# Optimization experiments

Measured on AMD Instinct MI355X. Metric: run time of the kernel, lower is better.

The kernel has to match this reference:

```python
import jax, jax.numpy as jnp
import numpy as np

N_QUBITS = 8
N_LAYERS = 2
DIM = 1 << N_QUBITS

# Precompute Pauli-Z eigenvalues per qubit (PennyLane: wire 0 = most significant bit)
_idx = np.arange(DIM)
_bits = ((_idx[None, :] >> (N_QUBITS - 1 - np.arange(N_QUBITS)[:, None])) & 1)  # [n, 2^n]
Z_EIG = jnp.asarray(1.0 - 2.0 * _bits, dtype=jnp.float32)                      # [n, 2^n]
# CZ diagonal signs for adjacent pairs (q, q+1)
CZ_SIGN = jnp.asarray(1.0 - 2.0 * (_bits[:-1] * _bits[1:]), dtype=jnp.float32)  # [n-1, 2^n]


def _rx(t):
    c = jnp.cos(0.5 * t).astype(jnp.complex64)
    s = jnp.sin(0.5 * t).astype(jnp.complex64)
    return jnp.stack([jnp.stack([c, -1j * s], -1), jnp.stack([-1j * s, c], -1)], -2)


def _ry(t):
    c = jnp.cos(0.5 * t).astype(jnp.complex64)
    s = jnp.sin(0.5 * t).astype(jnp.complex64)
    return jnp.stack([jnp.stack([c, -s], -1), jnp.stack([s, c], -1)], -2)


def _rz(t):
    e = jnp.exp(-0.5j * t.astype(jnp.complex64))
    z = jnp.zeros_like(e)
    return jnp.stack([jnp.stack([e, z], -1), jnp.stack([z, jnp.conj(e)], -1)], -2)


def _apply_1q(state, gate, q):
    # state: [B, 2^n]; gate: [B,2,2] (data-dependent angle) or [2,2] (shared weight)
    B = state.shape[0]
    L, R = 1 << q, 1 << (N_QUBITS - q - 1)
    st = state.reshape(B, L, 2, R)
    if gate.ndim == 3:
        st = jnp.einsum('bij,bljr->blir', gate, st)
    else:
        st = jnp.einsum('ij,bljr->blir', gate, st)
    return st.reshape(B, DIM)


def _circuit(angles, q_weights):
    # angles: [B, 3*n] real; q_weights: [n_layers, 2*n]
    B = angles.shape[0]
    state = jnp.zeros((B, DIM), dtype=jnp.complex64).at[:, 0].set(1.0)
    for l in range(N_LAYERS):
        for q in range(N_QUBITS):
            state = _apply_1q(state, _rx(angles[:, 3 * q]), q)
            state = _apply_1q(state, _ry(angles[:, 3 * q + 1]), q)
            state = _apply_1q(state, _rz(angles[:, 3 * q + 2]), q)
        for q in range(N_QUBITS):  # ansatz 1: hardware-efficient RY+RZ
            state = _apply_1q(state, _ry(q_weights[l, q]), q)
            state = _apply_1q(state, _rz(q_weights[l, q + N_QUBITS]), q)
        for q in range(N_QUBITS - 1):  # CZ chain (diagonal)
            state = state * CZ_SIGN[q]
    probs = state.real ** 2 + state.imag ** 2          # [B, 2^n]
    return probs @ Z_EIG.T                              # [B, n] expval PauliZ


def setup_inputs() -> dict:
    key = jax.random.key(0)
    ks = jax.random.split(key, 6)
    B = 8192
    return {
        'x': jax.random.normal(ks[0], (B, 64), dtype=jnp.float32),
        'W_adapter': jax.random.normal(ks[1], (3 * N_QUBITS, 64), dtype=jnp.float32) * 0.1,
        'b_adapter': jax.random.normal(ks[2], (3 * N_QUBITS,), dtype=jnp.float32) * 0.1,
        'q_weights': jax.random.normal(ks[3], (N_LAYERS, 2 * N_QUBITS), dtype=jnp.float32),
        'W_fc': jax.random.normal(ks[4], (1, N_QUBITS), dtype=jnp.float32) * 0.1,
        'b_fc': jax.random.normal(ks[5], (1,), dtype=jnp.float32) * 0.1,
    }


def reference(x, W_adapter, b_adapter, q_weights, W_fc, b_fc):
    angles = jnp.arctan(x @ W_adapter.T + b_adapter)   # [B, 3n]
    expvals = _circuit(angles, q_weights)              # [B, n]
    return expvals @ W_fc.T + b_fc                     # [B, 1]
```

## Files before the change

### kernel.cpp

```cpp
#include <hip/hip_runtime.h>
#include <math.h>

typedef __attribute__((ext_vector_type(2))) float f32x2;

__device__ __forceinline__ f32x2 sp(float s) { f32x2 v; v.x = s; v.y = s; return v; }

template <int CTRL, int RM, int BM>
__device__ __forceinline__ float dpp_add(float v) {
    int o = __builtin_amdgcn_update_dpp(0, __float_as_int(v), CTRL, RM, BM, true);
    return v + __int_as_float(o);
}

__device__ __forceinline__ float wave_total(float v) {
    v = dpp_add<0xB1, 0xF, 0xF>(v);
    v = dpp_add<0x4E, 0xF, 0xF>(v);
    v = dpp_add<0x114, 0xF, 0xE>(v);
    v = dpp_add<0x118, 0xF, 0xC>(v);
    v = dpp_add<0x142, 0xA, 0xF>(v);
    v = dpp_add<0x143, 0xC, 0xF>(v);
    return __int_as_float(__builtin_amdgcn_readlane(__float_as_int(v), 63));
}

__device__ __forceinline__ float read_lane(float v, int l) {
    return __int_as_float(__builtin_amdgcn_readlane(__float_as_int(v), l));
}

template <int P>
__device__ __forceinline__ float partner(float v) {
    int vi = __float_as_int(v);
    if constexpr (P == 0) {
        return __int_as_float(__builtin_amdgcn_update_dpp(vi, vi, 0xB1, 0xF, 0xF, false));
    } else if constexpr (P == 1) {
        return __int_as_float(__builtin_amdgcn_update_dpp(vi, vi, 0x4E, 0xF, 0xF, false));
    } else if constexpr (P == 2) {
        int a = __builtin_amdgcn_update_dpp(vi, vi, 0x104, 0xF, 0x5, false);
        a = __builtin_amdgcn_update_dpp(a, vi, 0x114, 0xF, 0xA, false);
        return __int_as_float(a);
    } else if constexpr (P == 3) {
        int a = __builtin_amdgcn_update_dpp(vi, vi, 0x108, 0xF, 0x3, false);
        a = __builtin_amdgcn_update_dpp(a, vi, 0x118, 0xF, 0xC, false);
        return __int_as_float(a);
    } else if constexpr (P == 4) {
        return __shfl_xor(v, 16, 64);
    } else {
        return __shfl_xor(v, 32, 64);
    }
}

template <int P>
__device__ __forceinline__ f32x2 partner2(f32x2 v) {
    f32x2 r; r.x = partner<P>(v.x); r.y = partner<P>(v.y); return r;
}

__device__ __forceinline__ void pair_gate(float& r0, float& i0, float& r1, float& i1,
                                          float ar, float ai, float br, float bi) {
    float nr0 = ar * r0 - ai * i0 - br * r1 - bi * i1;
    float ni0 = ar * i0 + ai * r0 + bi * r1 - br * i1;
    float nr1 = br * r0 - bi * i0 + ar * r1 + ai * i1;
    float ni1 = br * i0 + bi * r0 + ar * i1 - ai * r1;
    r0 = nr0; i0 = ni0; r1 = nr1; i1 = ni1;
}

__device__ __forceinline__ void pair_gate2(f32x2& r0, f32x2& i0, f32x2& r1, f32x2& i1,
                                           float ar, float ai, float br, float bi) {
    f32x2 va = sp(ar), vi = sp(ai), vb = sp(br), vc = sp(bi);
    f32x2 nr0 = va * r0 - vi * i0 - vb * r1 - vc * i1;
    f32x2 ni0 = va * i0 + vi * r0 + vc * r1 - vb * i1;
    f32x2 nr1 = vb * r0 - vc * i0 + va * r1 + vi * i1;
    f32x2 ni1 = vb * i0 + vc * r0 + va * i1 - vi * r1;
    r0 = nr0; i0 = ni0; r1 = nr1; i1 = ni1;
}

template <int P>
__device__ __forceinline__ void cross_gate(int lane, f32x2& Ar, f32x2& Ai, f32x2& Br, f32x2& Bi,
                                           float gar, float gai, float gbr, float gbi) {
    float sg = ((lane >> P) & 1) ? 1.0f : -1.0f;
    f32x2 vAr = sp(gar), vAi = sp(-sg * gai), vBr = sp(sg * gbr), vBi = sp(gbi);
    f32x2 pr = partner2<P>(Ar), pi = partner2<P>(Ai);
    f32x2 nAr = vAr * Ar - vAi * Ai + vBr * pr - vBi * pi;
    f32x2 nAi = vAr * Ai + vAi * Ar + vBr * pi + vBi * pr;
    Ar = nAr; Ai = nAi;
    pr = partner2<P>(Br); pi = partner2<P>(Bi);
    f32x2 nBr = vAr * Br - vAi * Bi + vBr * pr - vBi * pi;
    f32x2 nBi = vAr * Bi + vAi * Br + vBr * pi + vBi * pr;
    Br = nBr; Bi = nBi;
}

template <int G>
__device__ __forceinline__ void apply_g(int lane, f32x2& Ar, f32x2& Ai, f32x2& Br, f32x2& Bi,
                                        float garv, float gaiv, float gbrv, float gbiv) {
    constexpr int Q = G & 7;
    constexpr int P = 7 - Q;
    float ar = read_lane(garv, G), ai = read_lane(gaiv, G);
    float br = read_lane(gbrv, G), bi = read_lane(gbiv, G);
    if constexpr (P == 7) {
        pair_gate2(Ar, Ai, Br, Bi, ar, ai, br, bi);
    } else if constexpr (P == 6) {
        float r0 = Ar.x, i0 = Ai.x, r1 = Ar.y, i1 = Ai.y;
        pair_gate(r0, i0, r1, i1, ar, ai, br, bi);
        Ar.x = r0; Ai.x = i0; Ar.y = r1; Ai.y = i1;
        r0 = Br.x; i0 = Bi.x; r1 = Br.y; i1 = Bi.y;
        pair_gate(r0, i0, r1, i1, ar, ai, br, bi);
        Br.x = r0; Bi.x = i0; Br.y = r1; Bi.y = i1;
    } else {
        cross_gate<P>(lane, Ar, Ai, Br, Bi, ar, ai, br, bi);
    }
}

__global__ __launch_bounds__(256) void qcritic_kernel(
    const float* __restrict__ x,
    const float* __restrict__ Wad,
    const float* __restrict__ bad,
    const float* __restrict__ qw,
    const float* __restrict__ Wfc,
    const float* __restrict__ bfc,
    float* __restrict__ out,
    int B) {
    int tid = threadIdx.x;
    int lane = tid & 63;
    int b = blockIdx.x * 4 + (tid >> 6);
    if (b >= B) return;

    float xv = x[b * 64 + lane];
    float u[24];
#pragma unroll
    for (int j = 0; j < 24; ++j)
        u[j] = wave_total(xv * Wad[j * 64 + lane]) + bad[j];

    int Q = lane & 7;
    int L = (lane >> 3) & 1;
    bool b0 = Q & 1, b1 = Q & 2, b2 = Q & 4;
    float uq[3];
#pragma unroll
    for (int k = 0; k < 3; ++k) {
        float m01 = b0 ? u[3 + k] : u[0 + k];
        float m23 = b0 ? u[9 + k] : u[6 + k];
        float m45 = b0 ? u[15 + k] : u[12 + k];
        float m67 = b0 ? u[21 + k] : u[18 + k];
        float m03 = b1 ? m23 : m01;
        float m47 = b1 ? m67 : m45;
        uq[k] = b2 ? m47 : m03;
    }
    float ch[3], sh[3];
#pragma unroll
    for (int k = 0; k < 3; ++k) {
        float v = uq[k];
        float ct = rsqrtf(1.0f + v * v);
        ch[k] = sqrtf(0.5f * (1.0f + ct));
        sh[k] = __fdividef(0.5f * v * ct, ch[k]);
    }
    float cd, sd, wc, ws;
    __sincosf(0.5f * qw[(L << 4) + Q], &sd, &cd);
    __sincosf(0.5f * qw[(L << 4) + Q + 8], &ws, &wc);
    if (L == 1) { wc = 1.0f; ws = 0.0f; }
    float ca = ch[0], sa = sh[0], cb = ch[1], sb = sh[1], zc = ch[2], zs = sh[2];
    float pr = cb * ca, pi = sb * sa;
    float qr = sb * ca, qi = -cb * sa;
    float a1r = zc * pr + zs * pi, a1i = zc * pi - zs * pr;
    float b1r = zc * qr - zs * qi, b1i = zc * qi + zs * qr;
    float a2r = cd * a1r - sd * b1r, a2i = cd * a1i - sd * b1i;
    float b2r = sd * a1r + cd * b1r, b2i = sd * a1i + cd * b1i;
    float garv = wc * a2r + ws * a2i, gaiv = wc * a2i - ws * a2r;
    float gbrv = wc * b2r - ws * b2i, gbiv = wc * b2i + ws * b2r;

    f32x2 Ar, Ai, Br, Bi;
    Ar.x = (lane == 0) ? 1.0f : 0.0f; Ar.y = 0.0f;
    Ai = sp(0.0f); Br = sp(0.0f); Bi = sp(0.0f);

    f32x2 czA, czB;
    {
        int i0 = lane, i1 = 64 + lane, i2 = 128 + lane, i3 = 192 + lane;
        czA.x = (__popc(i0 & (i0 >> 1)) & 1) ? -1.0f : 1.0f;
        czA.y = (__popc(i1 & (i1 >> 1)) & 1) ? -1.0f : 1.0f;
        czB.x = (__popc(i2 & (i2 >> 1)) & 1) ? -1.0f : 1.0f;
        czB.y = (__popc(i3 & (i3 >> 1)) & 1) ? -1.0f : 1.0f;
    }

    apply_g<0>(lane, Ar, Ai, Br, Bi, garv, gaiv, gbrv, gbiv);
    apply_g<1>(lane, Ar, Ai, Br, Bi, garv, gaiv, gbrv, gbiv);
    apply_g<2>(lane, Ar, Ai, Br, Bi, garv, gaiv, gbrv, gbiv);
    apply_g<3>(lane, Ar, Ai, Br, Bi, garv, gaiv, gbrv, gbiv);
    apply_g<4>(lane, Ar, Ai, Br, Bi, garv, gaiv, gbrv, gbiv);
    apply_g<5>(lane, Ar, Ai, Br, Bi, garv, gaiv, gbrv, gbiv);
    apply_g<6>(lane, Ar, Ai, Br, Bi, garv, gaiv, gbrv, gbiv);
    apply_g<7>(lane, Ar, Ai, Br, Bi, garv, gaiv, gbrv, gbiv);
    Ar *= czA; Ai *= czA; Br *= czB; Bi *= czB;

    apply_g<8>(lane, Ar, Ai, Br, Bi, garv, gaiv, gbrv, gbiv);
    apply_g<9>(lane, Ar, Ai, Br, Bi, garv, gaiv, gbrv, gbiv);
    apply_g<10>(lane, Ar, Ai, Br, Bi, garv, gaiv, gbrv, gbiv);
    apply_g<11>(lane, Ar, Ai, Br, Bi, garv, gaiv, gbrv, gbiv);
    apply_g<12>(lane, Ar, Ai, Br, Bi, garv, gaiv, gbrv, gbiv);
    apply_g<13>(lane, Ar, Ai, Br, Bi, garv, gaiv, gbrv, gbiv);
    apply_g<14>(lane, Ar, Ai, Br, Bi, garv, gaiv, gbrv, gbiv);
    apply_g<15>(lane, Ar, Ai, Br, Bi, garv, gaiv, gbrv, gbiv);

    float glow = 0.0f;
#pragma unroll
    for (int k = 2; k < 8; ++k)
        glow += Wfc[k] * (((lane >> (7 - k)) & 1) ? -1.0f : 1.0f);
    float w0 = Wfc[0], w1 = Wfc[1];
    f32x2 gA, gB;
    gA.x = glow + w0 + w1; gA.y = glow + w0 - w1;
    gB.x = glow - w0 + w1; gB.y = glow - w0 - w1;
    f32x2 acc2 = (Ar * Ar + Ai * Ai) * gA + (Br * Br + Bi * Bi) * gB;
    float tot = wave_total(acc2.x + acc2.y);
    if (lane == 0) out[b] = tot + bfc[0];
}

extern "C" void kernel_launch(void* const* d_in, const int* in_sizes, int n_in,
                              void* d_out, int out_size, void* d_ws, size_t ws_size,
                              hipStream_t stream) {
    const float* x   = (const float*)d_in[0];
    const float* Wad = (const float*)d_in[1];
    const float* bad = (const float*)d_in[2];
    const float* qw  = (const float*)d_in[3];
    const float* Wfc = (const float*)d_in[4];
    const float* bfc = (const float*)d_in[5];
    float* out = (float*)d_out;
    int B = in_sizes[0] / 64;
    int grid = (B + 3) / 4;
    qcritic_kernel<<<grid, 256, 0, stream>>>(x, Wad, bad, qw, Wfc, bfc, out, B);
}
```

Before: 80.22 us.

## Add occupancy hint, hoist Wfc loads, move CZ sign compute, use precise math

Adds an 8-waves-per-EU launch bound and hoists the Wfc and bfc loads to the start of the kernel. It moves the CZ sign computation to the point where it is used, and makes the final reduction write from lane 63 instead of doing a readlane. It also swaps the fast intrinsics __sincosf and __fdividef for the precise sincosf and divide. The precise math paths cost more instructions, and the occupancy bound may force register spills.

```diff
diff --git a/kernel.cpp b/kernel.cpp
--- a/kernel.cpp
+++ b/kernel.cpp
@@ -11,14 +11,14 @@
     return v + __int_as_float(o);
 }
 
-__device__ __forceinline__ float wave_total(float v) {
+__device__ __forceinline__ float wave_sum63(float v) {
     v = dpp_add<0xB1, 0xF, 0xF>(v);
     v = dpp_add<0x4E, 0xF, 0xF>(v);
     v = dpp_add<0x114, 0xF, 0xE>(v);
     v = dpp_add<0x118, 0xF, 0xC>(v);
     v = dpp_add<0x142, 0xA, 0xF>(v);
     v = dpp_add<0x143, 0xC, 0xF>(v);
-    return __int_as_float(__builtin_amdgcn_readlane(__float_as_int(v), 63));
+    return v;
 }
 
 __device__ __forceinline__ float read_lane(float v, int l) {
@@ -107,7 +107,7 @@
     }
 }
 
-__global__ __launch_bounds__(256) void qcritic_kernel(
+__global__ __launch_bounds__(256, 8) void qcritic_kernel(
     const float* __restrict__ x,
     const float* __restrict__ Wad,
     const float* __restrict__ bad,
@@ -121,11 +121,20 @@
     int b = blockIdx.x * 4 + (tid >> 6);
     if (b >= B) return;
 
+    float w0 = Wfc[0], w1 = Wfc[1];
+    float glow = 0.0f;
+#pragma unroll
+    for (int k = 2; k < 8; ++k)
+        glow += Wfc[k] * (((lane >> (7 - k)) & 1) ? -1.0f : 1.0f);
+    float bfcv = bfc[0];
+
     float xv = x[b * 64 + lane];
-    float u[24];
-#pragma unroll
-    for (int j = 0; j < 24; ++j)
-        u[j] = wave_total(xv * Wad[j * 64 + lane]) + bad[j];
+    float su[24];
+#pragma unroll
+    for (int j = 0; j < 24; ++j) {
+        float p = wave_sum63(xv * Wad[j * 64 + lane]);
+        su[j] = read_lane(p, 63) + bad[j];
+    }
 
     int Q = lane & 7;
     int L = (lane >> 3) & 1;
@@ -133,10 +142,10 @@
     float uq[3];
 #pragma unroll
     for (int k = 0; k < 3; ++k) {
-        float m01 = b0 ? u[3 + k] : u[0 + k];
-        float m23 = b0 ? u[9 + k] : u[6 + k];
-        float m45 = b0 ? u[15 + k] : u[12 + k];
-        float m67 = b0 ? u[21 + k] : u[18 + k];
+        float m01 = b0 ? su[3 + k] : su[0 + k];
+        float m23 = b0 ? su[9 + k] : su[6 + k];
+        float m45 = b0 ? su[15 + k] : su[12 + k];
+        float m67 = b0 ? su[21 + k] : su[18 + k];
         float m03 = b1 ? m23 : m01;
         float m47 = b1 ? m67 : m45;
         uq[k] = b2 ? m47 : m03;
@@ -147,17 +156,17 @@
         float v = uq[k];
         float ct = rsqrtf(1.0f + v * v);
         ch[k] = sqrtf(0.5f * (1.0f + ct));
-        sh[k] = __fdividef(0.5f * v * ct, ch[k]);
+        sh[k] = 0.5f * v * ct / ch[k];
     }
     float cd, sd, wc, ws;
-    __sincosf(0.5f * qw[(L << 4) + Q], &sd, &cd);
-    __sincosf(0.5f * qw[(L << 4) + Q + 8], &ws, &wc);
+    sincosf(0.5f * qw[(L << 4) + Q], &sd, &cd);
+    sincosf(0.5f * qw[(L << 4) + Q + 8], &ws, &wc);
     if (L == 1) { wc = 1.0f; ws = 0.0f; }
     float ca = ch[0], sa = sh[0], cb = ch[1], sb = sh[1], zc = ch[2], zs = sh[2];
     float pr = cb * ca, pi = sb * sa;
-    float qr = sb * ca, qi = -cb * sa;
+    float qr = sb * ca, qi2 = -cb * sa;
     float a1r = zc * pr + zs * pi, a1i = zc * pi - zs * pr;
-    float b1r = zc * qr - zs * qi, b1i = zc * qi + zs * qr;
+    float b1r = zc * qr - zs * qi2, b1i = zc * qi2 + zs * qr;
     float a2r = cd * a1r - sd * b1r, a2i = cd * a1i - sd * b1i;
     float b2r = sd * a1r + cd * b1r, b2i = sd * a1i + cd * b1i;
     float garv = wc * a2r + ws * a2i, gaiv = wc * a2i - ws * a2r;
@@ -166,15 +175,6 @@
     f32x2 Ar, Ai, Br, Bi;
     Ar.x = (lane == 0) ? 1.0f : 0.0f; Ar.y = 0.0f;
     Ai = sp(0.0f); Br = sp(0.0f); Bi = sp(0.0f);
-
-    f32x2 czA, czB;
-    {
-        int i0 = lane, i1 = 64 + lane, i2 = 128 + lane, i3 = 192 + lane;
-        czA.x = (__popc(i0 & (i0 >> 1)) & 1) ? -1.0f : 1.0f;
-        czA.y = (__popc(i1 & (i1 >> 1)) & 1) ? -1.0f : 1.0f;
-        czB.x = (__popc(i2 & (i2 >> 1)) & 1) ? -1.0f : 1.0f;
-        czB.y = (__popc(i3 & (i3 >> 1)) & 1) ? -1.0f : 1.0f;
-    }
 
     apply_g<0>(lane, Ar, Ai, Br, Bi, garv, gaiv, gbrv, gbiv);
     apply_g<1>(lane, Ar, Ai, Br, Bi, garv, gaiv, gbrv, gbiv);
@@ -184,7 +184,16 @@
     apply_g<5>(lane, Ar, Ai, Br, Bi, garv, gaiv, gbrv, gbiv);
     apply_g<6>(lane, Ar, Ai, Br, Bi, garv, gaiv, gbrv, gbiv);
     apply_g<7>(lane, Ar, Ai, Br, Bi, garv, gaiv, gbrv, gbiv);
-    Ar *= czA; Ai *= czA; Br *= czB; Bi *= czB;
+
+    {
+        int i0 = lane, i1 = 64 + lane, i2 = 128 + lane, i3 = 192 + lane;
+        f32x2 czA, czB;
+        czA.x = (__popc(i0 & (i0 >> 1)) & 1) ? -1.0f : 1.0f;
+        czA.y = (__popc(i1 & (i1 >> 1)) & 1) ? -1.0f : 1.0f;
+        czB.x = (__popc(i2 & (i2 >> 1)) & 1) ? -1.0f : 1.0f;
+        czB.y = (__popc(i3 & (i3 >> 1)) & 1) ? -1.0f : 1.0f;
+        Ar *= czA; Ai *= czA; Br *= czB; Bi *= czB;
+    }
 
     apply_g<8>(lane, Ar, Ai, Br, Bi, garv, gaiv, gbrv, gbiv);
     apply_g<9>(lane, Ar, Ai, Br, Bi, garv, gaiv, gbrv, gbiv);
@@ -195,17 +204,12 @@
     apply_g<14>(lane, Ar, Ai, Br, Bi, garv, gaiv, gbrv, gbiv);
     apply_g<15>(lane, Ar, Ai, Br, Bi, garv, gaiv, gbrv, gbiv);
 
-    float glow = 0.0f;
-#pragma unroll
-    for (int k = 2; k < 8; ++k)
-        glow += Wfc[k] * (((lane >> (7 - k)) & 1) ? -1.0f : 1.0f);
-    float w0 = Wfc[0], w1 = Wfc[1];
     f32x2 gA, gB;
     gA.x = glow + w0 + w1; gA.y = glow + w0 - w1;
     gB.x = glow - w0 + w1; gB.y = glow - w0 - w1;
     f32x2 acc2 = (Ar * Ar + Ai * Ai) * gA + (Br * Br + Bi * Bi) * gB;
-    float tot = wave_total(acc2.x + acc2.y);
-    if (lane == 0) out[b] = tot + bfc[0];
+    float tot = wave_sum63(acc2.x + acc2.y);
+    if (lane == 63) out[b] = tot + bfcv;
 }
 
 extern "C" void kernel_launch(void* const* d_in, const int* in_sizes, int n_in,
```

Measured after the change: 80.73 us. Within noise of the previous version (+0.6%).
